# Performance work log

Hardware: AMD Instinct MI355X
Metric: run time of the kernel (lower is better)

The kernel has to match this reference:

```python
import jax, jax.numpy as jnp
import numpy as np

N = 65536      # total nodes = 64 graphs x 1024 nodes
B = 64         # graphs in batch
NPG = 1024     # nodes per graph
EPG = 16384    # edges per graph (avg degree 16)
H = 4          # attention heads
D = 32         # per-head out feats (graph_hiddens = [32, 32])
IN_DIM = 128
NEG_SLOPE = 0.2

def _glorot(key, shape):
    return jax.random.normal(key, shape, jnp.float32) / jnp.sqrt(jnp.float32(shape[0]))

def setup_inputs() -> dict:
    key = jax.random.key(0)
    ks = jax.random.split(key, 16)
    x = jax.random.normal(ks[0], (N, IN_DIM), jnp.float32)
    # edges generated within each graph: endpoint = graph_offset + local index
    offs = (jnp.arange(B, dtype=jnp.int32) * NPG)[:, None]
    src = (jax.random.randint(ks[1], (B, EPG), 0, NPG, jnp.int32) + offs).reshape(-1)
    dst = (jax.random.randint(ks[2], (B, EPG), 0, NPG, jnp.int32) + offs).reshape(-1)
    gid = jnp.repeat(jnp.arange(B, dtype=jnp.int32), NPG)
    return {
        "x": x, "src": src, "dst": dst, "gid": gid,
        # GATv2 layer 1 (in 128 -> H*D)
        "Ws1": _glorot(ks[3], (IN_DIM, H * D)), "bs1": jnp.zeros((H * D,), jnp.float32),
        "Wd1": _glorot(ks[4], (IN_DIM, H * D)), "bd1": jnp.zeros((H * D,), jnp.float32),
        "attn1": jax.random.normal(ks[5], (H, D), jnp.float32) * 0.1,
        # GATv2 layer 2 (in 32 -> H*D)
        "Ws2": _glorot(ks[6], (D, H * D)), "bs2": jnp.zeros((H * D,), jnp.float32),
        "Wd2": _glorot(ks[7], (D, H * D)), "bd2": jnp.zeros((H * D,), jnp.float32),
        "attn2": jax.random.normal(ks[8], (H, D), jnp.float32) * 0.1,
        # global attention pooling gate Linear(D, 1)
        "gW": _glorot(ks[9], (D, 1)), "gb": jnp.zeros((1,), jnp.float32),
    }

def gatv2_maxpool(h, src, dst, Ws, bs, Wd, bd, attn):
    """DGL GATv2Conv (share_weights=False, attn_drop=0/eval) + MaxPool1d over heads."""
    fs = (h @ Ws + bs).reshape(N, H, D)   # fc_src
    fd = (h @ Wd + bd).reshape(N, H, D)   # fc_dst
    e = jax.nn.leaky_relu(fs[src] + fd[dst], NEG_SLOPE)     # [E,H,D]
    s = jnp.einsum('ehd,hd->eh', e, attn)                    # per-edge logits [E,H]
    m = jax.lax.stop_gradient(jax.ops.segment_max(s, dst, num_segments=N))
    a = jnp.exp(s - m[dst])
    z = jax.ops.segment_sum(a, dst, num_segments=N)
    alpha = a / z[dst]                                       # edge softmax per dst node
    out = jax.ops.segment_sum(alpha[:, :, None] * fs[src], dst, num_segments=N)  # [N,H,D]
    return out.max(axis=1)                                   # maxpool over heads -> [N,D]

def reference(x, src, dst, gid, Ws1, bs1, Wd1, bd1, attn1, Ws2, bs2, Wd2, bd2, attn2, gW, gb):
    h = gatv2_maxpool(x, src, dst, Ws1, bs1, Wd1, bd1, attn1)
    h = gatv2_maxpool(h, src, dst, Ws2, bs2, Wd2, bd2, attn2)
    # GlobalAttentionPooling: softmax(gate) over nodes within each graph
    g = (h @ gW + gb)[:, 0]                                  # [N]
    gm = jax.lax.stop_gradient(jax.ops.segment_max(g, gid, num_segments=B))
    ga = jnp.exp(g - gm[gid])
    gz = jax.ops.segment_sum(ga, gid, num_segments=B)
    w = ga / gz[gid]
    return jax.ops.segment_sum(w[:, None] * h, gid, num_segments=B)  # [B,D]
```

## Files before the change

### kernel.cpp

```cpp
#include <hip/hip_runtime.h>
#include <hip/hip_fp16.h>
#include <math.h>

#define N_NODES 65536
#define B_GRAPHS 64
#define NPG 1024
#define EPG 16384
#define E_TOTAL (B_GRAPHS * EPG)
#define NEG 0.2f

typedef float f32x4 __attribute__((ext_vector_type(4)));
typedef _Float16 f16x8 __attribute__((ext_vector_type(8)));
typedef _Float16 h2v __attribute__((ext_vector_type(2)));
typedef int i32x4 __attribute__((ext_vector_type(4)));
typedef unsigned int uint32;
typedef unsigned short u16;

union FragH { i32x4 i; f16x8 h; uint32 u[4]; };
union H2U { uint32 u; h2v h; };

__device__ __forceinline__ float fast_exp2(float x) {
    float r;
    asm("v_exp_f32 %0, %1" : "=v"(r) : "v"(x));
    return r;
}

__device__ __forceinline__ uint32 f2h2(float a, float b) {
    __half2 h = __float22half2_rn(make_float2(a, b));
    return *(uint32*)&h;
}
__device__ __forceinline__ float2 h2f(uint32 u) {
    __half2 h = *(__half2*)&u;
    return __half22float2(h);
}

__device__ __forceinline__ void pk_fma_acc(uint32& acc, uint32 fv, uint32 pe2) {
    asm("v_pk_fma_f16 %0, %1, %2, %0" : "+v"(acc) : "v"(fv), "v"(pe2));
}

__device__ __forceinline__ float dot_term(uint32 fvu, h2v fdv, h2v neg2, h2v av, float accum) {
    H2U fv; fv.u = fvu;
    h2v e = fv.h + fdv;
    h2v en = e * neg2;
    h2v em;
    asm("v_pk_max_f16 %0, %1, %2" : "=v"(em) : "v"(e), "v"(en));
    float sp;
    asm("v_dot2_f32_f16 %0, %1, %2, %3" : "=v"(sp) : "v"(em), "v"(av), "v"(accum));
    return sp;
}

__global__ __launch_bounds__(1024) void k_prep(const int* __restrict__ src, const int* __restrict__ dst,
                                               int* __restrict__ rowptr, int* __restrict__ colb,
                                               int2* __restrict__ ndpack,
                                               const float* __restrict__ Ws1, const float* __restrict__ Wd1,
                                               const float* __restrict__ Ws2, const float* __restrict__ Wd2,
                                               __half* __restrict__ Wf1, __half* __restrict__ Wf2) {
    __shared__ int cnt[NPG];
    __shared__ int cur[NPG];
    __shared__ int scol[EPG];
    __shared__ int wsum[16];
    __shared__ int hd[64];
    __shared__ int hcur[64];
    if (blockIdx.x >= B_GRAPHS) {
        int id = (blockIdx.x - B_GRAPHS) * 1024 + threadIdx.x;
        if (id < 32768) {
            int j = id & 7, l = (id >> 3) & 63, c = (id >> 9) & 3, T = id >> 11;
            int k = c * 32 + (l >> 4) * 8 + j;
            int n = (T & 7) * 16 + (l & 15);
            const float* W = (T < 8) ? Ws1 : Wd1;
            Wf1[id] = __float2half_rn(W[k * 128 + n]);
        } else if (id < 40960) {
            int rem = id - 32768;
            int j = rem & 7, l = (rem >> 3) & 63, T = rem >> 9;
            int k = (l >> 4) * 8 + j;
            int n = (T & 7) * 16 + (l & 15);
            const float* W = (T < 8) ? Ws2 : Wd2;
            Wf2[rem] = __float2half_rn(W[k * 128 + n]);
        }
        return;
    }
    int g = blockIdx.x, tid = threadIdx.x;
    int lane = tid & 63, wid = tid >> 6;
    int ebase = g * EPG;
    cnt[tid] = 0;
    __syncthreads();
    for (int e = tid; e < EPG; e += 1024)
        atomicAdd(&cnt[dst[ebase + e] & (NPG - 1)], 1);
    __syncthreads();
    int deg0 = cnt[tid];
    int v = deg0;
#pragma unroll
    for (int off = 1; off < 64; off <<= 1) {
        int t = __shfl_up(v, off);
        if (lane >= off) v += t;
    }
    if (lane == 63) wsum[wid] = v;
    __syncthreads();
    if (tid < 16) {
        int sv = wsum[tid];
#pragma unroll
        for (int off = 1; off < 16; off <<= 1) {
            int t = __shfl_up(sv, off);
            if (tid >= off) sv += t;
        }
        wsum[tid] = sv;
    }
    __syncthreads();
    int excl = v + (wid ? wsum[wid - 1] : 0) - deg0;
    rowptr[g * NPG + tid] = ebase + excl;
    if (g == B_GRAPHS - 1 && tid == 0) rowptr[N_NODES] = E_TOTAL;
    cur[tid] = excl;
    __syncthreads();
    for (int e = tid; e < EPG; e += 1024) {
        int d = dst[ebase + e] & (NPG - 1);
        int p = atomicAdd(&cur[d], 1);
        scol[p] = src[ebase + e] << 9;
    }
    if (tid < 64) hd[tid] = 0;
    __syncthreads();
    int dc = deg0; dc = (dc > 63) ? 63 : dc;
    atomicAdd(&hd[dc], 1);
    int4* cg = (int4*)(colb + ebase);
    const int4* cs = (const int4*)scol;
    for (int i = tid; i < EPG / 4; i += 1024) cg[i] = cs[i];
    __syncthreads();
    if (tid == 0) {
        int run = 0;
#pragma unroll 8
        for (int i = 0; i < 64; ++i) { hcur[i] = run; run += hd[i]; }
    }
    __syncthreads();
    int pos = atomicAdd(&hcur[dc], 1);
    ndpack[g * NPG + pos] = make_int2(ebase + excl, (g * NPG + tid) | (deg0 << 16));
}

template <int K>
__global__ __launch_bounds__(512) void k_gemm_mfma(const float* __restrict__ X,
                                                   const __half* __restrict__ Wf,
                                                   const float* __restrict__ bs, const float* __restrict__ bd,
                                                   u16* __restrict__ fsd) {
    constexpr int NC = K / 32;
    constexpr int LDK = K + 8;
    __shared__ float xsbuf[4352];
    float* xs = xsbuf;
    u16* eb = (u16*)xsbuf;
    int tid = threadIdx.x;
    int lane = tid & 63, wv = tid >> 6;
    int l15 = lane & 15, kg = lane >> 4;
    int ng = wv & 1, Tb = (wv >> 1) * 4;
    int nb = blockIdx.x * 32;

    if (K == 128) {
#pragma unroll
        for (int j = 0; j < 2; ++j) {
            int f = tid + j * 512;
            int r = f >> 5, c4 = f & 31;
            *(float4*)(xs + r * LDK + c4 * 4) = *(const float4*)(X + (size_t)(nb + r) * K + c4 * 4);
        }
    } else {
        if (tid < 256) {
            int r = tid >> 3, c4 = tid & 7;
            *(float4*)(xs + r * LDK + c4 * 4) = *(const float4*)(X + (size_t)(nb + r) * K + c4 * 4);
        }
    }
    __syncthreads();

    int ridx = ng * 16 + l15;
    FragH xf[NC];
#pragma unroll
    for (int c = 0; c < NC; ++c) {
        const float* xr = xs + ridx * LDK + c * 32 + kg * 8;
        float4 v0 = *(const float4*)xr;
        float4 v1 = *(const float4*)(xr + 4);
        xf[c].u[0] = f2h2(v0.x, v0.y);
        xf[c].u[1] = f2h2(v0.z, v0.w);
        xf[c].u[2] = f2h2(v1.x, v1.y);
        xf[c].u[3] = f2h2(v1.z, v1.w);
    }

    f32x4 acc[4];
#pragma unroll
    for (int i = 0; i < 4; ++i) acc[i] = (f32x4){0.f, 0.f, 0.f, 0.f};

#pragma unroll
    for (int i = 0; i < 4; ++i) {
        int T = Tb + i;
        const __half* wp = Wf + ((size_t)(T * NC) * 64 + lane) * 8;
#pragma unroll
        for (int c = 0; c < NC; ++c) {
            FragH wfr;
            wfr.i = *(const i32x4*)(wp + (size_t)c * 512);
            acc[i] = __builtin_amdgcn_mfma_f32_16x16x32_f16(wfr.h, xf[c].h, acc[i], 0, 0, 0);
        }
    }
    __syncthreads();

#pragma unroll
    for (int i = 0; i < 4; ++i) {
        int T = Tb + i;
        const float* bp = (T < 8) ? bs : bd;
        float4 bv = *(const float4*)(bp + (T & 7) * 16 + kg * 4);
        uint2 pk;
        pk.x = f2h2(acc[i][0] + bv.x, acc[i][1] + bv.y);
        pk.y = f2h2(acc[i][2] + bv.z, acc[i][3] + bv.w);
        int colh = (T & 7) * 16 + (T >> 3) * 128 + kg * 4;
        *(uint2*)(eb + (ng * 16 + l15) * 264 + colh) = pk;
    }
    __syncthreads();

#pragma unroll
    for (int j = 0; j < 2; ++j) {
        int f = tid + j * 512;
        int r = f >> 5, c = f & 31;
        i32x4 v = *(const i32x4*)(eb + r * 264 + c * 8);
        *(i32x4*)(fsd + (size_t)(nb + r) * 256 + c * 8) = v;
    }
}

__global__ __launch_bounds__(256) void k_edge(const u16* __restrict__ fsd,
                                              const int* __restrict__ colb,
                                              const int2* __restrict__ ndpack,
                                              const float* __restrict__ attn, float* __restrict__ hout) {
    int w = threadIdx.x >> 6, lane = threadIdx.x & 63;
    int bid = blockIdx.x;
    int nb = (bid & 7) * 512 + (bid >> 3);
    int g2 = nb >> 6, bb = nb & 63;
    int q = lane >> 4, s = lane & 15;
    int wgl = bb * 4 + w;
    int quad = (wgl & 3) * 64 + (wgl >> 2);
    int2 nd = ndpack[g2 * NPG + quad * 4 + q];
    int start = nd.x;
    int n = nd.y & 0xFFFF;
    int deg = nd.y >> 16;
    const char* fsdb = (const char*)fsd;

    const float* ap = attn + (s >> 2) * 32 + (s & 3) * 8;
    float4 a0 = *(const float4*)ap;
    float4 a1 = *(const float4*)(ap + 4);
    const float L2E = 1.44269504089f;
    h2v av0, av1, av2, av3;
    { H2U t; t.u = f2h2(a0.x * L2E, a0.y * L2E); av0 = t.h;
      t.u = f2h2(a0.z * L2E, a0.w * L2E); av1 = t.h;
      t.u = f2h2(a1.x * L2E, a1.y * L2E); av2 = t.h;
      t.u = f2h2(a1.z * L2E, a1.w * L2E); av3 = t.h; }
    h2v neg2; neg2[0] = (_Float16)NEG; neg2[1] = (_Float16)NEG;

    i32x4 fdq = *(const i32x4*)(fsdb + ((size_t)n << 9) + 256 + (s << 4));
    H2U fd0, fd1, fd2, fd3;
    fd0.u = (uint32)fdq[0]; fd1.u = (uint32)fdq[1]; fd2.u = (uint32)fdq[2]; fd3.u = (uint32)fdq[3];

    int m = deg;
    { int t16 = __shfl_xor(m, 16); m = (t16 > m) ? t16 : m;
      int t32 = __shfl_xor(m, 32); m = (t32 > m) ? t32 : m; }
    int niter = (__builtin_amdgcn_readfirstlane(m) + 3) >> 2;

    const char* fb = fsdb + (s << 4);
    const int* cb = colb + start;

    float z = 0.f;
    uint32 c0 = 0, c1 = 0, c2 = 0, c3 = 0;

    auto gather = [&](uint32 cval) -> i32x4 {
        return *(const i32x4*)(fb + (cval & 0x01FFFE00u));
    };

    auto proc = [&](i32x4 f, int e) {
        uint32 w0 = (uint32)f[0], w1 = (uint32)f[1], w2 = (uint32)f[2], w3 = (uint32)f[3];
        float sp = dot_term(w0, fd0.h, neg2, av0, 0.f);
        sp = dot_term(w1, fd1.h, neg2, av1, sp);
        sp = dot_term(w2, fd2.h, neg2, av2, sp);
        sp = dot_term(w3, fd3.h, neg2, av3, sp);
        sp += __shfl_xor(sp, 1);
        sp += __shfl_xor(sp, 2);
        float pe = fast_exp2(sp);
        pe = (e < deg) ? pe : 0.f;
        z += pe;
        uint32 pe2 = f2h2(pe, pe);
        pk_fma_acc(c0, w0, pe2);
        pk_fma_acc(c1, w1, pe2);
        pk_fma_acc(c2, w2, pe2);
        pk_fma_acc(c3, w3, pe2);
    };

    uint32 cnxt0 = (uint32)cb[4], cnxt1 = (uint32)cb[5], cnxt2 = (uint32)cb[6], cnxt3 = (uint32)cb[7];
    i32x4 fv0 = gather((uint32)cb[0]), fv1 = gather((uint32)cb[1]),
          fv2 = gather((uint32)cb[2]), fv3 = gather((uint32)cb[3]);

    for (int k = 0; k < niter; ++k) {
        int e = k * 4;
        i32x4 a = fv0, b = fv1, c = fv2, d = fv3;
        fv0 = gather(cnxt0); fv1 = gather(cnxt1); fv2 = gather(cnxt2); fv3 = gather(cnxt3);
        cnxt0 = (uint32)cb[e + 8]; cnxt1 = (uint32)cb[e + 9];
        cnxt2 = (uint32)cb[e + 10]; cnxt3 = (uint32)cb[e + 11];
        proc(a, e + 0);
        proc(b, e + 1);
        proc(c, e + 2);
        proc(d, e + 3);
    }

    float2 u0 = h2f(c0), u1 = h2f(c1), u2 = h2f(c2), u3 = h2f(c3);
    float r = (z > 0.f) ? 1.f / z : 0.f;
    float d0 = u0.x * r, d1 = u0.y * r, d2 = u1.x * r, d3 = u1.y * r;
    float d4 = u2.x * r, d5 = u2.y * r, d6 = u3.x * r, d7 = u3.y * r;

    d0 = fmaxf(d0, __shfl_xor(d0, 4)); d0 = fmaxf(d0, __shfl_xor(d0, 8));
    d1 = fmaxf(d1, __shfl_xor(d1, 4)); d1 = fmaxf(d1, __shfl_xor(d1, 8));
    d2 = fmaxf(d2, __shfl_xor(d2, 4)); d2 = fmaxf(d2, __shfl_xor(d2, 8));
    d3 = fmaxf(d3, __shfl_xor(d3, 4)); d3 = fmaxf(d3, __shfl_xor(d3, 8));
    d4 = fmaxf(d4, __shfl_xor(d4, 4)); d4 = fmaxf(d4, __shfl_xor(d4, 8));
    d5 = fmaxf(d5, __shfl_xor(d5, 4)); d5 = fmaxf(d5, __shfl_xor(d5, 8));
    d6 = fmaxf(d6, __shfl_xor(d6, 4)); d6 = fmaxf(d6, __shfl_xor(d6, 8));
    d7 = fmaxf(d7, __shfl_xor(d7, 4)); d7 = fmaxf(d7, __shfl_xor(d7, 8));

    if (s < 4) {
        float* op = hout + ((size_t)n << 5) + (s << 3);
        *(float4*)op = make_float4(d0, d1, d2, d3);
        *(float4*)(op + 4) = make_float4(d4, d5, d6, d7);
    }
}

__global__ __launch_bounds__(256) void k_pool(const float* __restrict__ h2, const float* __restrict__ gW,
                                              const float* __restrict__ gb, float* __restrict__ out) {
    int b = blockIdx.x, tid = threadIdx.x;
    __shared__ float ga[NPG];
    __shared__ float red[256];
    __shared__ float gws[32];
    const float* hb = h2 + (size_t)b * NPG * 32;
    if (tid < 32) gws[tid] = gW[tid];
    __syncthreads();
    float gbv = gb[0];
    float lmax = -INFINITY;
    float gloc[4];
#pragma unroll
    for (int j = 0; j < 4; ++j) {
        int nl = tid + j * 256;
        const float* row = hb + nl * 32;
        float dot = 0.f;
#pragma unroll
        for (int c = 0; c < 32; c += 4) {
            float4 v = *(const float4*)(row + c);
            dot += v.x * gws[c] + v.y * gws[c + 1] + v.z * gws[c + 2] + v.w * gws[c + 3];
        }
        gloc[j] = dot + gbv;
        lmax = fmaxf(lmax, gloc[j]);
    }
    red[tid] = lmax; __syncthreads();
    for (int s2 = 128; s2 > 0; s2 >>= 1) { if (tid < s2) red[tid] = fmaxf(red[tid], red[tid + s2]); __syncthreads(); }
    float m = red[0];
    __syncthreads();
    float lsum = 0.f;
#pragma unroll
    for (int j = 0; j < 4; ++j) {
        int nl = tid + j * 256;
        float a = __expf(gloc[j] - m);
        ga[nl] = a;
        lsum += a;
    }
    red[tid] = lsum; __syncthreads();
    for (int s2 = 128; s2 > 0; s2 >>= 1) { if (tid < s2) red[tid] += red[tid + s2]; __syncthreads(); }
    float z = red[0];
    __syncthreads();
    int d = tid & 31, ng = tid >> 5;
    float acc = 0.f;
    for (int nl = ng; nl < NPG; nl += 8) acc += ga[nl] * hb[nl * 32 + d];
    red[tid] = acc; __syncthreads();
    if (tid < 32) {
        float s = red[tid];
#pragma unroll
        for (int g2 = 1; g2 < 8; ++g2) s += red[g2 * 32 + tid];
        out[b * 32 + tid] = s / z;
    }
}

extern "C" void kernel_launch(void* const* d_in, const int* in_sizes, int n_in,
                              void* d_out, int out_size, void* d_ws, size_t ws_size,
                              hipStream_t stream) {
    const float* x     = (const float*)d_in[0];
    const int*   src   = (const int*)d_in[1];
    const int*   dst   = (const int*)d_in[2];
    const float* Ws1   = (const float*)d_in[4];
    const float* bs1   = (const float*)d_in[5];
    const float* Wd1   = (const float*)d_in[6];
    const float* bd1   = (const float*)d_in[7];
    const float* attn1 = (const float*)d_in[8];
    const float* Ws2   = (const float*)d_in[9];
    const float* bs2   = (const float*)d_in[10];
    const float* Wd2   = (const float*)d_in[11];
    const float* bd2   = (const float*)d_in[12];
    const float* attn2 = (const float*)d_in[13];
    const float* gW    = (const float*)d_in[14];
    const float* gb    = (const float*)d_in[15];
    float* out = (float*)d_out;

    u16* fsd   = (u16*)d_ws;
    float* h1  = (float*)(fsd + (size_t)N_NODES * 256);
    float* h2  = h1 + (size_t)N_NODES * 32;
    int* rowptr = (int*)(h2 + (size_t)N_NODES * 32);
    int* colb   = rowptr + (N_NODES + 4);
    __half* Wf1 = (__half*)(colb + E_TOTAL);
    __half* Wf2 = Wf1 + 32768;
    int2* ndpack = (int2*)(Wf2 + 8192);

    k_prep<<<B_GRAPHS + 40, 1024, 0, stream>>>(src, dst, rowptr, colb, ndpack,
                                               Ws1, Wd1, Ws2, Wd2, Wf1, Wf2);

    k_gemm_mfma<128><<<N_NODES / 32, 512, 0, stream>>>(x, Wf1, bs1, bd1, fsd);
    k_edge<<<N_NODES / 16, 256, 0, stream>>>(fsd, colb, ndpack, attn1, h1);

    k_gemm_mfma<32><<<N_NODES / 32, 512, 0, stream>>>(h1, Wf2, bs2, bd2, fsd);
    k_edge<<<N_NODES / 16, 256, 0, stream>>>(fsd, colb, ndpack, attn2, h2);

    k_pool<<<B_GRAPHS, 256, 0, stream>>>(h2, gW, gb, out);
}
```

Measured before the change: 129.7 us.

## Process two degree-paired node quads per wave and split unmasked edge loop

Each wave now handles two groups of four destination nodes, picked from opposite ends of the degree-sorted order (wgl and 255-wgl), so total work per wave is balanced, and the edge kernel launches half as many blocks. The per-quad loop is split into a full-iteration phase without degree masking, using the lane-0 degree as minimum, and a masked tail up to the lane-48 degree as maximum. This relies on ndpack being sorted by degree within each quad. It reduces masking work and tail imbalance but halves the number of waves available to hide gather latency.

```diff
diff --git a/kernel.cpp b/kernel.cpp
--- a/kernel.cpp
+++ b/kernel.cpp
@@ -223,16 +223,17 @@
                                               const float* __restrict__ attn, float* __restrict__ hout) {
     int w = threadIdx.x >> 6, lane = threadIdx.x & 63;
     int bid = blockIdx.x;
-    int nb = (bid & 7) * 512 + (bid >> 3);
-    int g2 = nb >> 6, bb = nb & 63;
+    int nb = (bid & 7) * 256 + (bid >> 3);
+    int g2 = nb >> 5, bb = nb & 31;
     int q = lane >> 4, s = lane & 15;
     int wgl = bb * 4 + w;
-    int quad = (wgl & 3) * 64 + (wgl >> 2);
-    int2 nd = ndpack[g2 * NPG + quad * 4 + q];
-    int start = nd.x;
-    int n = nd.y & 0xFFFF;
-    int deg = nd.y >> 16;
+    const int2* npg = ndpack + g2 * NPG;
+    int2 ndA = npg[wgl * 4 + q];
+    int2 ndB = npg[(255 - wgl) * 4 + q];
     const char* fsdb = (const char*)fsd;
+    int nA = ndA.y & 0xFFFF, nB = ndB.y & 0xFFFF;
+    i32x4 fdqA = *(const i32x4*)(fsdb + ((size_t)nA << 9) + 256 + (s << 4));
+    i32x4 fdqB = *(const i32x4*)(fsdb + ((size_t)nB << 9) + 256 + (s << 4));
 
     const float* ap = attn + (s >> 2) * 32 + (s & 3) * 8;
     float4 a0 = *(const float4*)ap;
@@ -244,79 +245,96 @@
       t.u = f2h2(a1.x * L2E, a1.y * L2E); av2 = t.h;
       t.u = f2h2(a1.z * L2E, a1.w * L2E); av3 = t.h; }
     h2v neg2; neg2[0] = (_Float16)NEG; neg2[1] = (_Float16)NEG;
-
-    i32x4 fdq = *(const i32x4*)(fsdb + ((size_t)n << 9) + 256 + (s << 4));
-    H2U fd0, fd1, fd2, fd3;
-    fd0.u = (uint32)fdq[0]; fd1.u = (uint32)fdq[1]; fd2.u = (uint32)fdq[2]; fd3.u = (uint32)fdq[3];
-
-    int m = deg;
-    { int t16 = __shfl_xor(m, 16); m = (t16 > m) ? t16 : m;
-      int t32 = __shfl_xor(m, 32); m = (t32 > m) ? t32 : m; }
-    int niter = (__builtin_amdgcn_readfirstlane(m) + 3) >> 2;
-
     const char* fb = fsdb + (s << 4);
-    const int* cb = colb + start;
-
-    float z = 0.f;
-    uint32 c0 = 0, c1 = 0, c2 = 0, c3 = 0;
-
-    auto gather = [&](uint32 cval) -> i32x4 {
-        return *(const i32x4*)(fb + (cval & 0x01FFFE00u));
+
+    auto runQuad = [&](int2 nd, i32x4 fdq) {
+        int start = nd.x;
+        int n = nd.y & 0xFFFF;
+        int deg = nd.y >> 16;
+        H2U fd0, fd1, fd2, fd3;
+        fd0.u = (uint32)fdq[0]; fd1.u = (uint32)fdq[1]; fd2.u = (uint32)fdq[2]; fd3.u = (uint32)fdq[3];
+        int dmin = __builtin_amdgcn_readlane(deg, 0);
+        int dmax = __builtin_amdgcn_readlane(deg, 48);
+        int nfull = dmin >> 2;
+        int niter = (dmax + 3) >> 2;
+        const int* cb = colb + start;
+
+        float z = 0.f;
+        uint32 c0 = 0, c1 = 0, c2 = 0, c3 = 0;
+
+        auto gather = [&](uint32 cval) -> i32x4 {
+            return *(const i32x4*)(fb + (cval & 0x01FFFE00u));
+        };
+        auto edge_core = [&](i32x4 f) -> float {
+            uint32 w0 = (uint32)f[0], w1 = (uint32)f[1], w2 = (uint32)f[2], w3 = (uint32)f[3];
+            float sp = dot_term(w0, fd0.h, neg2, av0, 0.f);
+            sp = dot_term(w1, fd1.h, neg2, av1, sp);
+            sp = dot_term(w2, fd2.h, neg2, av2, sp);
+            sp = dot_term(w3, fd3.h, neg2, av3, sp);
+            sp += __shfl_xor(sp, 1);
+            sp += __shfl_xor(sp, 2);
+            return fast_exp2(sp);
+        };
+        auto accum = [&](i32x4 f, float pe) {
+            z += pe;
+            uint32 pe2 = f2h2(pe, pe);
+            pk_fma_acc(c0, (uint32)f[0], pe2);
+            pk_fma_acc(c1, (uint32)f[1], pe2);
+            pk_fma_acc(c2, (uint32)f[2], pe2);
+            pk_fma_acc(c3, (uint32)f[3], pe2);
+        };
+
+        uint32 cnxt0 = (uint32)cb[4], cnxt1 = (uint32)cb[5], cnxt2 = (uint32)cb[6], cnxt3 = (uint32)cb[7];
+        i32x4 fv0 = gather((uint32)cb[0]), fv1 = gather((uint32)cb[1]),
+              fv2 = gather((uint32)cb[2]), fv3 = gather((uint32)cb[3]);
+
+        int k = 0;
+        for (; k < nfull; ++k) {
+            int e = k * 4;
+            i32x4 a = fv0, b = fv1, c = fv2, d = fv3;
+            fv0 = gather(cnxt0); fv1 = gather(cnxt1); fv2 = gather(cnxt2); fv3 = gather(cnxt3);
+            cnxt0 = (uint32)cb[e + 8]; cnxt1 = (uint32)cb[e + 9];
+            cnxt2 = (uint32)cb[e + 10]; cnxt3 = (uint32)cb[e + 11];
+            accum(a, edge_core(a));
+            accum(b, edge_core(b));
+            accum(c, edge_core(c));
+            accum(d, edge_core(d));
+        }
+        for (; k < niter; ++k) {
+            int e = k * 4;
+            i32x4 a = fv0, b = fv1, c = fv2, d = fv3;
+            fv0 = gather(cnxt0); fv1 = gather(cnxt1); fv2 = gather(cnxt2); fv3 = gather(cnxt3);
+            cnxt0 = (uint32)cb[e + 8]; cnxt1 = (uint32)cb[e + 9];
+            cnxt2 = (uint32)cb[e + 10]; cnxt3 = (uint32)cb[e + 11];
+            float pa = edge_core(a); accum(a, (e + 0 < deg) ? pa : 0.f);
+            float pb = edge_core(b); accum(b, (e + 1 < deg) ? pb : 0.f);
+            float pc = edge_core(c); accum(c, (e + 2 < deg) ? pc : 0.f);
+            float pd = edge_core(d); accum(d, (e + 3 < deg) ? pd : 0.f);
+        }
+
+        float2 u0 = h2f(c0), u1 = h2f(c1), u2 = h2f(c2), u3 = h2f(c3);
+        float r = (z > 0.f) ? 1.f / z : 0.f;
+        float d0 = u0.x * r, d1 = u0.y * r, d2 = u1.x * r, d3 = u1.y * r;
+        float d4 = u2.x * r, d5 = u2.y * r, d6 = u3.x * r, d7 = u3.y * r;
+
+        d0 = fmaxf(d0, __shfl_xor(d0, 4)); d0 = fmaxf(d0, __shfl_xor(d0, 8));
+        d1 = fmaxf(d1, __shfl_xor(d1, 4)); d1 = fmaxf(d1, __shfl_xor(d1, 8));
+        d2 = fmaxf(d2, __shfl_xor(d2, 4)); d2 = fmaxf(d2, __shfl_xor(d2, 8));
+        d3 = fmaxf(d3, __shfl_xor(d3, 4)); d3 = fmaxf(d3, __shfl_xor(d3, 8));
+        d4 = fmaxf(d4, __shfl_xor(d4, 4)); d4 = fmaxf(d4, __shfl_xor(d4, 8));
+        d5 = fmaxf(d5, __shfl_xor(d5, 4)); d5 = fmaxf(d5, __shfl_xor(d5, 8));
+        d6 = fmaxf(d6, __shfl_xor(d6, 4)); d6 = fmaxf(d6, __shfl_xor(d6, 8));
+        d7 = fmaxf(d7, __shfl_xor(d7, 4)); d7 = fmaxf(d7, __shfl_xor(d7, 8));
+
+        if (s < 4) {
+            float* op = hout + ((size_t)n << 5) + (s << 3);
+            *(float4*)op = make_float4(d0, d1, d2, d3);
+            *(float4*)(op + 4) = make_float4(d4, d5, d6, d7);
+        }
     };
 
-    auto proc = [&](i32x4 f, int e) {
-        uint32 w0 = (uint32)f[0], w1 = (uint32)f[1], w2 = (uint32)f[2], w3 = (uint32)f[3];
-        float sp = dot_term(w0, fd0.h, neg2, av0, 0.f);
-        sp = dot_term(w1, fd1.h, neg2, av1, sp);
-        sp = dot_term(w2, fd2.h, neg2, av2, sp);
-        sp = dot_term(w3, fd3.h, neg2, av3, sp);
-        sp += __shfl_xor(sp, 1);
-        sp += __shfl_xor(sp, 2);
-        float pe = fast_exp2(sp);
-        pe = (e < deg) ? pe : 0.f;
-        z += pe;
-        uint32 pe2 = f2h2(pe, pe);
-        pk_fma_acc(c0, w0, pe2);
-        pk_fma_acc(c1, w1, pe2);
-        pk_fma_acc(c2, w2, pe2);
-        pk_fma_acc(c3, w3, pe2);
-    };
-
-    uint32 cnxt0 = (uint32)cb[4], cnxt1 = (uint32)cb[5], cnxt2 = (uint32)cb[6], cnxt3 = (uint32)cb[7];
-    i32x4 fv0 = gather((uint32)cb[0]), fv1 = gather((uint32)cb[1]),
-          fv2 = gather((uint32)cb[2]), fv3 = gather((uint32)cb[3]);
-
-    for (int k = 0; k < niter; ++k) {
-        int e = k * 4;
-        i32x4 a = fv0, b = fv1, c = fv2, d = fv3;
-        fv0 = gather(cnxt0); fv1 = gather(cnxt1); fv2 = gather(cnxt2); fv3 = gather(cnxt3);
-        cnxt0 = (uint32)cb[e + 8]; cnxt1 = (uint32)cb[e + 9];
-        cnxt2 = (uint32)cb[e + 10]; cnxt3 = (uint32)cb[e + 11];
-        proc(a, e + 0);
-        proc(b, e + 1);
-        proc(c, e + 2);
-        proc(d, e + 3);
-    }
-
-    float2 u0 = h2f(c0), u1 = h2f(c1), u2 = h2f(c2), u3 = h2f(c3);
-    float r = (z > 0.f) ? 1.f / z : 0.f;
-    float d0 = u0.x * r, d1 = u0.y * r, d2 = u1.x * r, d3 = u1.y * r;
-    float d4 = u2.x * r, d5 = u2.y * r, d6 = u3.x * r, d7 = u3.y * r;
-
-    d0 = fmaxf(d0, __shfl_xor(d0, 4)); d0 = fmaxf(d0, __shfl_xor(d0, 8));
-    d1 = fmaxf(d1, __shfl_xor(d1, 4)); d1 = fmaxf(d1, __shfl_xor(d1, 8));
-    d2 = fmaxf(d2, __shfl_xor(d2, 4)); d2 = fmaxf(d2, __shfl_xor(d2, 8));
-    d3 = fmaxf(d3, __shfl_xor(d3, 4)); d3 = fmaxf(d3, __shfl_xor(d3, 8));
-    d4 = fmaxf(d4, __shfl_xor(d4, 4)); d4 = fmaxf(d4, __shfl_xor(d4, 8));
-    d5 = fmaxf(d5, __shfl_xor(d5, 4)); d5 = fmaxf(d5, __shfl_xor(d5, 8));
-    d6 = fmaxf(d6, __shfl_xor(d6, 4)); d6 = fmaxf(d6, __shfl_xor(d6, 8));
-    d7 = fmaxf(d7, __shfl_xor(d7, 4)); d7 = fmaxf(d7, __shfl_xor(d7, 8));
-
-    if (s < 4) {
-        float* op = hout + ((size_t)n << 5) + (s << 3);
-        *(float4*)op = make_float4(d0, d1, d2, d3);
-        *(float4*)(op + 4) = make_float4(d4, d5, d6, d7);
-    }
+    runQuad(ndA, fdqA);
+    runQuad(ndB, fdqB);
 }
 
 __global__ __launch_bounds__(256) void k_pool(const float* __restrict__ h2, const float* __restrict__ gW,
@@ -405,10 +423,10 @@
                                                Ws1, Wd1, Ws2, Wd2, Wf1, Wf2);
 
     k_gemm_mfma<128><<<N_NODES / 32, 512, 0, stream>>>(x, Wf1, bs1, bd1, fsd);
-    k_edge<<<N_NODES / 16, 256, 0, stream>>>(fsd, colb, ndpack, attn1, h1);
+    k_edge<<<N_NODES / 32, 256, 0, stream>>>(fsd, colb, ndpack, attn1, h1);
 
     k_gemm_mfma<32><<<N_NODES / 32, 512, 0, stream>>>(h1, Wf2, bs2, bd2, fsd);
-    k_edge<<<N_NODES / 16, 256, 0, stream>>>(fsd, colb, ndpack, attn2, h2);
+    k_edge<<<N_NODES / 32, 256, 0, stream>>>(fsd, colb, ndpack, attn2, h2);
 
     k_pool<<<B_GRAPHS, 256, 0, stream>>>(h2, gW, gb, out);
 }
```

After: 133.7 us. +3.1%, slower.
